# Kernel optimization log

Measured on AMD Instinct MI355X. Metric: run time of the kernel, lower is better.

## Reference

```python
import jax, jax.numpy as jnp
import numpy as np

B, T, H, CIN, COUT = 32, 16384, 64, 1, 1


def setup_inputs() -> dict:
    key = jax.random.key(0)
    ks = jax.random.split(key, 7)
    s = 1.0 / np.sqrt(H)  # torch default init bound for GRU / Linear(H, .)
    u = lambda k, shp: jax.random.uniform(k, shp, jnp.float32, -s, s)
    return {
        "x": jax.random.normal(ks[0], (B, T, CIN), jnp.float32),
        "W_ih": u(ks[1], (3 * H, CIN)),   # GRU weight_ih_l0 (r,z,n stacked)
        "W_hh": u(ks[2], (3 * H, H)),     # GRU weight_hh_l0
        "b_ih": u(ks[3], (3 * H,)),
        "b_hh": u(ks[4], (3 * H,)),
        "W_out": u(ks[5], (COUT, H)),     # linear head
        "b_out": u(ks[6], (COUT,)),
    }


def _gru_forward(x, W_ih, W_hh, b_ih, b_hh):
    # Precompute input projections for all timesteps (vectorized GEMM),
    # then scan the small hidden recurrence.
    x_proj = jnp.einsum('btc,gc->btg', x, W_ih) + b_ih     # [B,T,3H]
    x_proj = jnp.swapaxes(x_proj, 0, 1)                    # [T,B,3H]
    h0 = jnp.zeros((x.shape[0], H), x.dtype)

    def step(h, xp):
        gh = h @ W_hh.T + b_hh                             # [B,3H]
        r = jax.nn.sigmoid(xp[:, :H] + gh[:, :H])
        z = jax.nn.sigmoid(xp[:, H:2 * H] + gh[:, H:2 * H])
        n = jnp.tanh(xp[:, 2 * H:] + r * gh[:, 2 * H:])
        h_new = (1.0 - z) * n + z * h                      # torch GRU update
        return h_new, h_new

    h_last, states = jax.lax.scan(step, h0, x_proj)        # states: [T,B,H]
    return jnp.swapaxes(states, 0, 1), h_last              # [B,T,H], [B,H]


def reference(x, W_ih, W_hh, b_ih, b_hh, W_out, b_out):
    states, h_last = _gru_forward(x, W_ih, W_hh, b_ih, b_hh)
    out = states @ W_out.T + b_out                         # [B,T,1]
    out = out + x[..., 0:1]                                # residual connection
    return (out, states)
```

## Files before the change

kernel.cpp:

```cpp
#include <hip/hip_runtime.h>


#define Bv   32
#define Tv   16384
#define Hv   64

__device__ __forceinline__ float bcast(float v, int k) {
    return __int_as_float(__builtin_amdgcn_readlane(__float_as_int(v), k));
}

__device__ __forceinline__ void lds_barrier() {
    asm volatile("s_waitcnt lgkmcnt(0)" ::: "memory");
    __builtin_amdgcn_s_barrier();
    asm volatile("" ::: "memory");
}

#define DOT4(ACC, W, K)                                   \
    do {                                                  \
        ACC = fmaf(W.x, bcast(h, (K) + 0), ACC);          \
        ACC = fmaf(W.y, bcast(h, (K) + 1), ACC);          \
        ACC = fmaf(W.z, bcast(h, (K) + 2), ACC);          \
        ACC = fmaf(W.w, bcast(h, (K) + 3), ACC);          \
    } while (0)

__global__ __launch_bounds__(192, 1) void gru_scan(
    const float* __restrict__ x,
    const float* __restrict__ W_ih,
    const float* __restrict__ W_hh,
    const float* __restrict__ b_ih,
    const float* __restrict__ b_hh,
    float* __restrict__ states)
{
    const int b   = blockIdx.x;
    const int tid = threadIdx.x;
    const int wv  = tid >> 6;
    const int u   = tid & 63;
    const int g   = (wv << 6) + u;

    __shared__ float ghs[2][3][Hv];

    const float* xb = x + (size_t)b * Tv;
    float*       sb = states + (size_t)b * Tv * Hv;

    const float4* Wv = reinterpret_cast<const float4*>(W_hh + (size_t)g * Hv);
    const float4 w0  = Wv[0],  w1  = Wv[1],  w2  = Wv[2],  w3  = Wv[3];
    const float4 w4  = Wv[4],  w5  = Wv[5],  w6  = Wv[6],  w7  = Wv[7];
    const float4 w8  = Wv[8],  w9  = Wv[9],  w10 = Wv[10], w11 = Wv[11];
    const float4 w12 = Wv[12], w13 = Wv[13], w14 = Wv[14], w15 = Wv[15];
    const float bhh_g = b_hh[g];

    const float wih_r = W_ih[u];
    const float wih_z = W_ih[64  + u];
    const float wih_n = W_ih[128 + u];
    const float bih_r = b_ih[u];
    const float bih_z = b_ih[64  + u];
    const float bih_n = b_ih[128 + u];

    float h  = 0.0f;
    float xv = xb[u];

    for (int t0 = 0; t0 < Tv; t0 += 64) {
        const int tn = (t0 + 64 < Tv) ? (t0 + 64) : 0;
        const float xv_next = xb[tn + u];

#pragma unroll 2
        for (int tt = 0; tt < 64; ++tt) {
            const int pb = tt & 1;

            float a0 = bhh_g, a1 = 0.0f, a2 = 0.0f, a3 = 0.0f;
            DOT4(a0, w0,   0); DOT4(a1, w1,   4); DOT4(a2, w2,   8); DOT4(a3, w3,  12);
            DOT4(a0, w4,  16); DOT4(a1, w5,  20); DOT4(a2, w6,  24); DOT4(a3, w7,  28);
            DOT4(a0, w8,  32); DOT4(a1, w9,  36); DOT4(a2, w10, 40); DOT4(a3, w11, 44);
            DOT4(a0, w12, 48); DOT4(a1, w13, 52); DOT4(a2, w14, 56); DOT4(a3, w15, 60);
            ghs[pb][wv][u] = (a0 + a1) + (a2 + a3);

            const float xt  = bcast(xv, tt);
            const float ir  = fmaf(xt, wih_r, bih_r);
            const float iz  = fmaf(xt, wih_z, bih_z);
            const float in_ = fmaf(xt, wih_n, bih_n);

            lds_barrier();

            const float gr = ghs[pb][0][u];
            const float gz = ghs[pb][1][u];
            const float gn = ghs[pb][2][u];

            const float r  = 1.0f / (1.0f + __expf(-(ir + gr)));
            const float z  = 1.0f / (1.0f + __expf(-(iz + gz)));
            const float a  = fmaf(r, gn, in_);
            const float e  = __expf(2.0f * a);
            const float n  = 1.0f - 2.0f / (e + 1.0f);
            h = fmaf(z, h - n, n);

            if (wv == 0) sb[(size_t)(t0 + tt) * Hv + u] = h;
        }
        xv = xv_next;
    }
}

__global__ __launch_bounds__(256) void gru_head(
    const float* __restrict__ x,
    const float* __restrict__ states,
    const float* __restrict__ W_out,
    const float* __restrict__ b_out,
    float* __restrict__ out)
{
    __shared__ float wsm[Hv];
    if (threadIdx.x < Hv) wsm[threadIdx.x] = W_out[threadIdx.x];
    __syncthreads();

    const int i = blockIdx.x * blockDim.x + threadIdx.x;
    if (i >= Bv * Tv) return;

    const float4* s4 = reinterpret_cast<const float4*>(states + (size_t)i * Hv);
    float acc = 0.0f;
#pragma unroll
    for (int k = 0; k < Hv / 4; ++k) {
        const float4 v = s4[k];
        acc = fmaf(v.x, wsm[4*k+0], acc);
        acc = fmaf(v.y, wsm[4*k+1], acc);
        acc = fmaf(v.z, wsm[4*k+2], acc);
        acc = fmaf(v.w, wsm[4*k+3], acc);
    }
    out[i] = acc + b_out[0] + x[i];
}

extern "C" void kernel_launch(void* const* d_in, const int* in_sizes, int n_in,
                              void* d_out, int out_size, void* d_ws, size_t ws_size,
                              hipStream_t stream) {
    const float* x     = (const float*)d_in[0];
    const float* W_ih  = (const float*)d_in[1];
    const float* W_hh  = (const float*)d_in[2];
    const float* b_ih  = (const float*)d_in[3];
    const float* b_hh  = (const float*)d_in[4];
    const float* W_out = (const float*)d_in[5];
    const float* b_out = (const float*)d_in[6];

    float* out    = (float*)d_out;
    float* states = out + (size_t)Bv * Tv;

    gru_scan<<<Bv, 192, 0, stream>>>(x, W_ih, W_hh, b_ih, b_hh, states);
    gru_head<<<(Bv * Tv + 255) / 256, 256, 0, stream>>>(x, states, W_out, b_out, out);
}
```

Before: 6.791 ms.

## Process two batch rows per block to interleave independent GRU recurrences

Each scan block now advances two batch sequences in lockstep, sharing the register-resident W_hh rows and a single LDS barrier per timestep. The interleaved independent dot products and gate computations are meant to hide readlane/FMA, transcendental and barrier latency on the serial critical path. Half as many blocks are launched, and per-step instruction count roughly doubles, so an issue-bound loop could get longer.

```diff
diff --git a/kernel.cpp b/kernel.cpp
--- a/kernel.cpp
+++ b/kernel.cpp
@@ -15,12 +15,12 @@
     asm volatile("" ::: "memory");
 }
 
-#define DOT4(ACC, W, K)                                   \
+#define DOT4(ACC, W, H, K)                                \
     do {                                                  \
-        ACC = fmaf(W.x, bcast(h, (K) + 0), ACC);          \
-        ACC = fmaf(W.y, bcast(h, (K) + 1), ACC);          \
-        ACC = fmaf(W.z, bcast(h, (K) + 2), ACC);          \
-        ACC = fmaf(W.w, bcast(h, (K) + 3), ACC);          \
+        ACC = fmaf(W.x, bcast(H, (K) + 0), ACC);          \
+        ACC = fmaf(W.y, bcast(H, (K) + 1), ACC);          \
+        ACC = fmaf(W.z, bcast(H, (K) + 2), ACC);          \
+        ACC = fmaf(W.w, bcast(H, (K) + 3), ACC);          \
     } while (0)
 
 __global__ __launch_bounds__(192, 1) void gru_scan(
@@ -31,16 +31,18 @@
     const float* __restrict__ b_hh,
     float* __restrict__ states)
 {
-    const int b   = blockIdx.x;
+    const int b0  = blockIdx.x << 1;
     const int tid = threadIdx.x;
     const int wv  = tid >> 6;
     const int u   = tid & 63;
     const int g   = (wv << 6) + u;
 
-    __shared__ float ghs[2][3][Hv];
+    __shared__ float ghs[2][2][3][Hv];
 
-    const float* xb = x + (size_t)b * Tv;
-    float*       sb = states + (size_t)b * Tv * Hv;
+    const float* xbA = x + (size_t)b0 * Tv;
+    const float* xbB = x + (size_t)(b0 + 1) * Tv;
+    float*       sbA = states + (size_t)b0 * Tv * Hv;
+    float*       sbB = states + (size_t)(b0 + 1) * Tv * Hv;
 
     const float4* Wv = reinterpret_cast<const float4*>(W_hh + (size_t)g * Hv);
     const float4 w0  = Wv[0],  w1  = Wv[1],  w2  = Wv[2],  w3  = Wv[3];
@@ -56,45 +58,76 @@
     const float bih_z = b_ih[64  + u];
     const float bih_n = b_ih[128 + u];
 
-    float h  = 0.0f;
-    float xv = xb[u];
+    float hA = 0.0f, hB = 0.0f;
+    float xvA = xbA[u], xvB = xbB[u];
 
     for (int t0 = 0; t0 < Tv; t0 += 64) {
         const int tn = (t0 + 64 < Tv) ? (t0 + 64) : 0;
-        const float xv_next = xb[tn + u];
+        const float xvA_next = xbA[tn + u];
+        const float xvB_next = xbB[tn + u];
 
 #pragma unroll 2
         for (int tt = 0; tt < 64; ++tt) {
             const int pb = tt & 1;
 
-            float a0 = bhh_g, a1 = 0.0f, a2 = 0.0f, a3 = 0.0f;
-            DOT4(a0, w0,   0); DOT4(a1, w1,   4); DOT4(a2, w2,   8); DOT4(a3, w3,  12);
-            DOT4(a0, w4,  16); DOT4(a1, w5,  20); DOT4(a2, w6,  24); DOT4(a3, w7,  28);
-            DOT4(a0, w8,  32); DOT4(a1, w9,  36); DOT4(a2, w10, 40); DOT4(a3, w11, 44);
-            DOT4(a0, w12, 48); DOT4(a1, w13, 52); DOT4(a2, w14, 56); DOT4(a3, w15, 60);
-            ghs[pb][wv][u] = (a0 + a1) + (a2 + a3);
+            float aA0 = bhh_g, aA1 = 0.0f, aA2 = 0.0f, aA3 = 0.0f;
+            float aB0 = bhh_g, aB1 = 0.0f, aB2 = 0.0f, aB3 = 0.0f;
+            DOT4(aA0, w0,  hA,  0); DOT4(aB0, w0,  hB,  0);
+            DOT4(aA1, w1,  hA,  4); DOT4(aB1, w1,  hB,  4);
+            DOT4(aA2, w2,  hA,  8); DOT4(aB2, w2,  hB,  8);
+            DOT4(aA3, w3,  hA, 12); DOT4(aB3, w3,  hB, 12);
+            DOT4(aA0, w4,  hA, 16); DOT4(aB0, w4,  hB, 16);
+            DOT4(aA1, w5,  hA, 20); DOT4(aB1, w5,  hB, 20);
+            DOT4(aA2, w6,  hA, 24); DOT4(aB2, w6,  hB, 24);
+            DOT4(aA3, w7,  hA, 28); DOT4(aB3, w7,  hB, 28);
+            DOT4(aA0, w8,  hA, 32); DOT4(aB0, w8,  hB, 32);
+            DOT4(aA1, w9,  hA, 36); DOT4(aB1, w9,  hB, 36);
+            DOT4(aA2, w10, hA, 40); DOT4(aB2, w10, hB, 40);
+            DOT4(aA3, w11, hA, 44); DOT4(aB3, w11, hB, 44);
+            DOT4(aA0, w12, hA, 48); DOT4(aB0, w12, hB, 48);
+            DOT4(aA1, w13, hA, 52); DOT4(aB1, w13, hB, 52);
+            DOT4(aA2, w14, hA, 56); DOT4(aB2, w14, hB, 56);
+            DOT4(aA3, w15, hA, 60); DOT4(aB3, w15, hB, 60);
+            ghs[pb][0][wv][u] = (aA0 + aA1) + (aA2 + aA3);
+            ghs[pb][1][wv][u] = (aB0 + aB1) + (aB2 + aB3);
 
-            const float xt  = bcast(xv, tt);
-            const float ir  = fmaf(xt, wih_r, bih_r);
-            const float iz  = fmaf(xt, wih_z, bih_z);
-            const float in_ = fmaf(xt, wih_n, bih_n);
+            const float xtA  = bcast(xvA, tt);
+            const float irA  = fmaf(xtA, wih_r, bih_r);
+            const float izA  = fmaf(xtA, wih_z, bih_z);
+            const float inA  = fmaf(xtA, wih_n, bih_n);
+            const float xtB  = bcast(xvB, tt);
+            const float irB  = fmaf(xtB, wih_r, bih_r);
+            const float izB  = fmaf(xtB, wih_z, bih_z);
+            const float inB  = fmaf(xtB, wih_n, bih_n);
 
             lds_barrier();
 
-            const float gr = ghs[pb][0][u];
-            const float gz = ghs[pb][1][u];
-            const float gn = ghs[pb][2][u];
+            const float grA = ghs[pb][0][0][u];
+            const float gzA = ghs[pb][0][1][u];
+            const float gnA = ghs[pb][0][2][u];
+            const float grB = ghs[pb][1][0][u];
+            const float gzB = ghs[pb][1][1][u];
+            const float gnB = ghs[pb][1][2][u];
 
-            const float r  = 1.0f / (1.0f + __expf(-(ir + gr)));
-            const float z  = 1.0f / (1.0f + __expf(-(iz + gz)));
-            const float a  = fmaf(r, gn, in_);
-            const float e  = __expf(2.0f * a);
-            const float n  = 1.0f - 2.0f / (e + 1.0f);
-            h = fmaf(z, h - n, n);
+            const float rA = 1.0f / (1.0f + __expf(-(irA + grA)));
+            const float zA = 1.0f / (1.0f + __expf(-(izA + gzA)));
+            const float aA = fmaf(rA, gnA, inA);
+            const float eA = __expf(2.0f * aA);
+            const float nA = 1.0f - 2.0f / (eA + 1.0f);
+            hA = fmaf(zA, hA - nA, nA);
 
-            if (wv == 0) sb[(size_t)(t0 + tt) * Hv + u] = h;
+            const float rB = 1.0f / (1.0f + __expf(-(irB + grB)));
+            const float zB = 1.0f / (1.0f + __expf(-(izB + gzB)));
+            const float aB = fmaf(rB, gnB, inB);
+            const float eB = __expf(2.0f * aB);
+            const float nB = 1.0f - 2.0f / (eB + 1.0f);
+            hB = fmaf(zB, hB - nB, nB);
+
+            if (wv == 0)      sbA[(size_t)(t0 + tt) * Hv + u] = hA;
+            else if (wv == 1) sbB[(size_t)(t0 + tt) * Hv + u] = hB;
         }
-        xv = xv_next;
+        xvA = xvA_next;
+        xvB = xvB_next;
     }
 }
 
@@ -139,6 +172,6 @@
     float* out    = (float*)d_out;
     float* states = out + (size_t)Bv * Tv;
 
-    gru_scan<<<Bv, 192, 0, stream>>>(x, W_ih, W_hh, b_ih, b_hh, states);
+    gru_scan<<<Bv / 2, 192, 0, stream>>>(x, W_ih, W_hh, b_ih, b_hh, states);
     gru_head<<<(Bv * Tv + 255) / 256, 256, 0, stream>>>(x, states, W_out, b_out, out);
 }
```

New measurement: 19.83 ms. 192% more time.

## Split recurrent matvec K dimension across two waves per gate

Applied to the files above, without the earlier changes.

The block grows from 3 to 6 waves, so each gate section's 64-term hidden dot product is split into two 32-term halves, one per wave. The halves are summed after the LDS barrier. This halves the serial chain of readlane broadcasts and FMAs per timestep, which dominates the latency-bound recurrence. In exchange, six waves share four SIMDs, the barrier spans more waves, and every step does extra LDS reads and adds.

```diff
diff --git a/kernel.cpp b/kernel.cpp
--- a/kernel.cpp
+++ b/kernel.cpp
@@ -4,8 +4,10 @@
 #define Bv   32
 #define Tv   16384
 #define Hv   64
+#define NW   6
+#define NT   (NW * 64)
 
-__device__ __forceinline__ float bcast(float v, int k) {
+__device__ __forceinline__ float bcastf(float v, int k) {
     return __int_as_float(__builtin_amdgcn_readlane(__float_as_int(v), k));
 }
 
@@ -17,13 +19,13 @@
 
 #define DOT4(ACC, W, K)                                   \
     do {                                                  \
-        ACC = fmaf(W.x, bcast(h, (K) + 0), ACC);          \
-        ACC = fmaf(W.y, bcast(h, (K) + 1), ACC);          \
-        ACC = fmaf(W.z, bcast(h, (K) + 2), ACC);          \
-        ACC = fmaf(W.w, bcast(h, (K) + 3), ACC);          \
+        ACC = fmaf(W.x, bcastf(h, (K) + 0), ACC);         \
+        ACC = fmaf(W.y, bcastf(h, (K) + 1), ACC);         \
+        ACC = fmaf(W.z, bcastf(h, (K) + 2), ACC);         \
+        ACC = fmaf(W.w, bcastf(h, (K) + 3), ACC);         \
     } while (0)
 
-__global__ __launch_bounds__(192, 1) void gru_scan(
+__global__ __launch_bounds__(NT, 1) void gru_scan(
     const float* __restrict__ x,
     const float* __restrict__ W_ih,
     const float* __restrict__ W_hh,
@@ -35,19 +37,20 @@
     const int tid = threadIdx.x;
     const int wv  = tid >> 6;
     const int u   = tid & 63;
-    const int g   = (wv << 6) + u;
+    const int sec = wv >> 1;
+    const int kh  = wv & 1;
+    const int g   = (sec << 6) + u;
+    const int kb  = kh << 5;
 
-    __shared__ float ghs[2][3][Hv];
+    __shared__ float ghs[2][NW][Hv];
 
     const float* xb = x + (size_t)b * Tv;
     float*       sb = states + (size_t)b * Tv * Hv;
 
-    const float4* Wv = reinterpret_cast<const float4*>(W_hh + (size_t)g * Hv);
-    const float4 w0  = Wv[0],  w1  = Wv[1],  w2  = Wv[2],  w3  = Wv[3];
-    const float4 w4  = Wv[4],  w5  = Wv[5],  w6  = Wv[6],  w7  = Wv[7];
-    const float4 w8  = Wv[8],  w9  = Wv[9],  w10 = Wv[10], w11 = Wv[11];
-    const float4 w12 = Wv[12], w13 = Wv[13], w14 = Wv[14], w15 = Wv[15];
-    const float bhh_g = b_hh[g];
+    const float4* Wv = reinterpret_cast<const float4*>(W_hh + (size_t)g * Hv + kb);
+    const float4 w0 = Wv[0], w1 = Wv[1], w2 = Wv[2], w3 = Wv[3];
+    const float4 w4 = Wv[4], w5 = Wv[5], w6 = Wv[6], w7 = Wv[7];
+    const float bhh = (kh == 0) ? b_hh[g] : 0.0f;
 
     const float wih_r = W_ih[u];
     const float wih_z = W_ih[64  + u];
@@ -67,23 +70,23 @@
         for (int tt = 0; tt < 64; ++tt) {
             const int pb = tt & 1;
 
-            float a0 = bhh_g, a1 = 0.0f, a2 = 0.0f, a3 = 0.0f;
-            DOT4(a0, w0,   0); DOT4(a1, w1,   4); DOT4(a2, w2,   8); DOT4(a3, w3,  12);
-            DOT4(a0, w4,  16); DOT4(a1, w5,  20); DOT4(a2, w6,  24); DOT4(a3, w7,  28);
-            DOT4(a0, w8,  32); DOT4(a1, w9,  36); DOT4(a2, w10, 40); DOT4(a3, w11, 44);
-            DOT4(a0, w12, 48); DOT4(a1, w13, 52); DOT4(a2, w14, 56); DOT4(a3, w15, 60);
+            float a0 = bhh, a1 = 0.0f, a2 = 0.0f, a3 = 0.0f;
+            DOT4(a0, w0, kb +  0); DOT4(a1, w1, kb +  4);
+            DOT4(a2, w2, kb +  8); DOT4(a3, w3, kb + 12);
+            DOT4(a0, w4, kb + 16); DOT4(a1, w5, kb + 20);
+            DOT4(a2, w6, kb + 24); DOT4(a3, w7, kb + 28);
             ghs[pb][wv][u] = (a0 + a1) + (a2 + a3);
 
-            const float xt  = bcast(xv, tt);
+            const float xt  = bcastf(xv, tt);
             const float ir  = fmaf(xt, wih_r, bih_r);
             const float iz  = fmaf(xt, wih_z, bih_z);
             const float in_ = fmaf(xt, wih_n, bih_n);
 
             lds_barrier();
 
-            const float gr = ghs[pb][0][u];
-            const float gz = ghs[pb][1][u];
-            const float gn = ghs[pb][2][u];
+            const float gr = ghs[pb][0][u] + ghs[pb][1][u];
+            const float gz = ghs[pb][2][u] + ghs[pb][3][u];
+            const float gn = ghs[pb][4][u] + ghs[pb][5][u];
 
             const float r  = 1.0f / (1.0f + __expf(-(ir + gr)));
             const float z  = 1.0f / (1.0f + __expf(-(iz + gz)));
@@ -139,6 +142,6 @@
     float* out    = (float*)d_out;
     float* states = out + (size_t)Bv * Tv;
 
-    gru_scan<<<Bv, 192, 0, stream>>>(x, W_ih, W_hh, b_ih, b_hh, states);
+    gru_scan<<<Bv, NT, 0, stream>>>(x, W_ih, W_hh, b_ih, b_hh, states);
     gru_head<<<(Bv * Tv + 255) / 256, 256, 0, stream>>>(x, states, W_out, b_out, out);
 }
```

After: 12.13 ms. 78.5% more time.
